# Kernel optimization log

Measured on AMD Instinct MI355X. Metric: run time of the kernel, lower is better.

The kernel has to match this reference:

```python
import jax, jax.numpy as jnp
import numpy as np

N = 100000   # nodes
E = 1600000  # edges
IN = 128     # in_feats
H = 3        # num_heads
D = 16       # out_feats per head
K = 3        # hops
NEG_SLOPE = 0.2
EPS = 1e-9


def leaky(x):
    return jnp.where(x >= 0, x, NEG_SLOPE * x)


def segment_softmax(e, idx, n):
    # e: [E, H] scores, softmax over edges sharing the same idx (node)
    m = jax.ops.segment_max(e, idx, num_segments=n)
    ex = jnp.exp(e - m[idx])
    s = jax.ops.segment_sum(ex, idx, num_segments=n)
    return ex / s[idx]


def feat_trans(h, i, norm_scales, offsets, pos_emb):
    # per-hop mean/var normalization (biased var) + position embedding
    mean = h.mean(axis=-1, keepdims=True)
    var = h.var(axis=-1, keepdims=True) + EPS
    h = (h - mean) * norm_scales[i] * jax.lax.rsqrt(var) + offsets[i]
    return h + pos_emb[:, :, i, :]


def setup_inputs() -> dict:
    key = jax.random.key(0)
    ks = jax.random.split(key, 10)
    s = 0.1
    feat = jax.random.normal(ks[0], (N, IN), jnp.float32)
    src = jax.random.randint(ks[1], (E,), 0, N)
    dst = jax.random.randint(ks[2], (E,), 0, N)
    fc_W = jax.random.normal(ks[3], (IN, H * D), jnp.float32) * s
    attn_l = jax.random.normal(ks[4], (1, H, D), jnp.float32) * s
    attn_r = jax.random.normal(ks[5], (1, H, D), jnp.float32) * s
    hop_attn_l = jax.random.normal(ks[6], (1, H, D), jnp.float32) * s
    hop_attn_r = jax.random.normal(ks[7], (1, H, D), jnp.float32) * s
    pos_emb = jax.random.normal(ks[8], (1, H, K + 1, D), jnp.float32) * s
    norm_scales = jnp.ones((K + 1, 1, H, D), jnp.float32)
    offsets = jnp.zeros((K + 1, 1, H, D), jnp.float32)
    bias = jnp.zeros((H * D,), jnp.float32)
    return dict(feat=feat, src=src, dst=dst, fc_W=fc_W, attn_l=attn_l,
                attn_r=attn_r, hop_attn_l=hop_attn_l, hop_attn_r=hop_attn_r,
                pos_emb=pos_emb, norm_scales=norm_scales, offsets=offsets,
                bias=bias)


def reference(feat, src, dst, fc_W, attn_l, attn_r, hop_attn_l, hop_attn_r,
              pos_emb, norm_scales, offsets, bias):
    ft = (feat @ fc_W).reshape(N, H, D)            # [N,H,D]
    el = (ft * attn_l).sum(-1)                      # [N,H]
    er = (ft * attn_r).sum(-1)                      # [N,H]
    e = leaky(el[src] + er[dst])                    # [E,H]
    a_dst = jnp.clip(segment_softmax(e, dst, N), EPS, None)
    a_src = jnp.clip(segment_softmax(e, src, N), EPS, None)
    a = jnp.sqrt(a_dst * a_src)                     # [E,H] symmetric attention

    h_query = feat_trans(ft, 0, norm_scales, offsets, pos_emb)[:, :, None, :]
    hstack = []
    cur = ft
    for k in range(1, K + 1):
        msg = cur[src] * a[:, :, None]              # [E,H,D]
        cur = jax.ops.segment_sum(msg, dst, num_segments=N)
        hstack.append(feat_trans(cur, k, norm_scales, offsets, pos_emb))
    hstack = jnp.stack(hstack, axis=2)              # [N,H,K,D]

    # hop attention (weight_style='HA')
    astack = (hstack * hop_attn_r[:, :, None, :]).sum(-1, keepdims=True) \
           + (h_query * hop_attn_l[:, :, None, :]).sum(-1, keepdims=True)
    astack = jax.nn.softmax(leaky(astack), axis=2)  # [N,H,K,1]
    rst = (hstack * astack).sum(axis=2)             # [N,H,D]
    return rst + bias.reshape(1, H, D)
```

## Files before the change

kernel.cpp:

```cpp
#include <hip/hip_runtime.h>
#include <hip/hip_bf16.h>

typedef __hip_bfloat16 bf16;

#define N_NODES 100000
#define N_EDGES 1600000
#define IN_F    128
#define HH      3
#define DD      16
#define HD      48
#define NEG_SLOPE 0.2f
#define EPS_V   1e-9f

#define NB      391
#define BW_SH   8
#define MS_T    8192

__device__ __forceinline__ float leaky(float x) { return x >= 0.f ? x : NEG_SLOPE * x; }
__device__ __forceinline__ float b2f(bf16 x) { return __bfloat162float(x); }

__global__ __launch_bounds__(256) void k_gemm(const float* __restrict__ feat,
                                              const float* __restrict__ W,
                                              float* __restrict__ ft,
                                              bf16* __restrict__ ft16) {
    int row = blockIdx.x * 256 + threadIdx.x;
    if (row >= N_NODES) return;
    float acc[HD];
#pragma unroll
    for (int c = 0; c < HD; ++c) acc[c] = 0.f;
    const float4* frow = (const float4*)(feat + (size_t)row * IN_F);
    for (int k4 = 0; k4 < IN_F / 4; ++k4) {
        float4 f = frow[k4];
        int k = k4 * 4;
#pragma unroll
        for (int c = 0; c < HD; ++c) acc[c] += f.x * W[(k + 0) * HD + c];
#pragma unroll
        for (int c = 0; c < HD; ++c) acc[c] += f.y * W[(k + 1) * HD + c];
#pragma unroll
        for (int c = 0; c < HD; ++c) acc[c] += f.z * W[(k + 2) * HD + c];
#pragma unroll
        for (int c = 0; c < HD; ++c) acc[c] += f.w * W[(k + 3) * HD + c];
    }
    float4* orow = (float4*)(ft + (size_t)row * HD);
#pragma unroll
    for (int c = 0; c < HD / 4; ++c)
        orow[c] = make_float4(acc[4 * c], acc[4 * c + 1], acc[4 * c + 2], acc[4 * c + 3]);
    bf16* o16 = ft16 + (size_t)row * HD;
#pragma unroll
    for (int c = 0; c < HD; ++c) o16[c] = __float2bfloat16(acc[c]);
}

__global__ void k_eler(const float* __restrict__ ft, const float* __restrict__ attn_l,
                       const float* __restrict__ attn_r, float* __restrict__ el,
                       float* __restrict__ er) {
    int i = blockIdx.x * blockDim.x + threadIdx.x;
    if (i >= N_NODES * HH) return;
    int h = i % HH;
    float sl = 0.f, sr = 0.f;
#pragma unroll
    for (int d = 0; d < DD; ++d) {
        float v = ft[i * DD + d];
        sl += v * attn_l[h * DD + d];
        sr += v * attn_r[h * DD + d];
    }
    el[i] = sl;
    er[i] = sr;
}

__global__ __launch_bounds__(256) void k_bhist(const int4* __restrict__ src4,
                                               const int4* __restrict__ dst4,
                                               int* __restrict__ bcnt_s,
                                               int* __restrict__ bcnt_d) {
    __shared__ int ls[NB], ld_[NB];
    int t = threadIdx.x;
    for (int i = t; i < NB; i += 256) { ls[i] = 0; ld_[i] = 0; }
    __syncthreads();
    const int NE4 = N_EDGES / 4;
    for (int e = blockIdx.x * 256 + t; e < NE4; e += gridDim.x * 256) {
        int4 d = dst4[e];
        atomicAdd(&ld_[d.x >> BW_SH], 1);
        atomicAdd(&ld_[d.y >> BW_SH], 1);
        atomicAdd(&ld_[d.z >> BW_SH], 1);
        atomicAdd(&ld_[d.w >> BW_SH], 1);
        int4 s = src4[e];
        atomicAdd(&ls[s.x >> BW_SH], 1);
        atomicAdd(&ls[s.y >> BW_SH], 1);
        atomicAdd(&ls[s.z >> BW_SH], 1);
        atomicAdd(&ls[s.w >> BW_SH], 1);
    }
    __syncthreads();
    for (int i = t; i < NB; i += 256) {
        if (ld_[i]) atomicAdd(&bcnt_d[i], ld_[i]);
        if (ls[i]) atomicAdd(&bcnt_s[i], ls[i]);
    }
}

__global__ __launch_bounds__(512) void k_bscan(const int* __restrict__ bcnt_d,
                                               int* __restrict__ bbase_d,
                                               const int* __restrict__ bcnt_s,
                                               int* __restrict__ bbase_s,
                                               int* __restrict__ rows_d,
                                               int* __restrict__ rows_s) {
    __shared__ int buf[512];
    const int* c = blockIdx.x ? bcnt_s : bcnt_d;
    int* o = blockIdx.x ? bbase_s : bbase_d;
    int t = threadIdx.x;
    int v = (t < NB) ? c[t] : 0;
    buf[t] = v;
    __syncthreads();
    for (int off = 1; off < 512; off <<= 1) {
        int u = (t >= off) ? buf[t - off] : 0;
        __syncthreads();
        buf[t] += u;
        __syncthreads();
    }
    if (t < NB) o[t] = buf[t] - v;
    if (t == NB - 1) o[NB] = buf[t];
    if (t == 0) {
        if (blockIdx.x) rows_s[N_NODES] = N_EDGES;
        else            rows_d[N_NODES] = N_EDGES;
    }
}

__global__ __launch_bounds__(256) void k_msplit(const int* __restrict__ src,
                                                const int* __restrict__ dst,
                                                const int* __restrict__ bbase_d,
                                                const int* __restrict__ bbase_s,
                                                int* __restrict__ bfill_d,
                                                int* __restrict__ bfill_s,
                                                unsigned* __restrict__ bkt_d,
                                                unsigned* __restrict__ bkt_s) {
    __shared__ int lcD[NB], lcS[NB], wbD[NB], wbS[NB], rkD[NB], rkS[NB];
    int t = threadIdx.x;
    int e0 = blockIdx.x * MS_T;
    int e1 = min(e0 + MS_T, N_EDGES);
    for (int i = t; i < NB; i += 256) { lcD[i] = 0; lcS[i] = 0; rkD[i] = 0; rkS[i] = 0; }
    __syncthreads();
    for (int e = e0 + t; e < e1; e += 256) {
        atomicAdd(&lcD[dst[e] >> BW_SH], 1);
        atomicAdd(&lcS[src[e] >> BW_SH], 1);
    }
    __syncthreads();
    for (int i = t; i < NB; i += 256) {
        wbD[i] = bbase_d[i] + (lcD[i] ? atomicAdd(&bfill_d[i], lcD[i]) : 0);
        wbS[i] = bbase_s[i] + (lcS[i] ? atomicAdd(&bfill_s[i], lcS[i]) : 0);
    }
    __syncthreads();
    for (int e = e0 + t; e < e1; e += 256) {
        int s = src[e], d = dst[e];
        int bd = d >> BW_SH, bs = s >> BW_SH;
        int rd = atomicAdd(&rkD[bd], 1);
        int rs = atomicAdd(&rkS[bs], 1);
        bkt_d[wbD[bd] + rd] = (unsigned)s | ((unsigned)(d & 255) << 17);
        bkt_s[wbS[bs] + rs] = (unsigned)d | ((unsigned)(s & 255) << 17);
    }
}

__global__ __launch_bounds__(256) void k_bfinal(const unsigned* __restrict__ bkt,
                                                const int* __restrict__ bbase,
                                                int* __restrict__ rows,
                                                int* __restrict__ outarr) {
    __shared__ int cnt[256], pre[256], rnk[256], wsum[4];
    int b = blockIdx.x, t = threadIdx.x;
    int base = bbase[b], end = bbase[b + 1];
    cnt[t] = 0; rnk[t] = 0;
    __syncthreads();
    for (int i = base + t; i < end; i += 256)
        atomicAdd(&cnt[(bkt[i] >> 17) & 255], 1);
    __syncthreads();
    int lane = t & 63, w = t >> 6;
    int v = cnt[t];
    int sc = v;
#pragma unroll
    for (int off = 1; off < 64; off <<= 1) {
        int u = __shfl_up(sc, off, 64);
        if (lane >= off) sc += u;
    }
    if (lane == 63) wsum[w] = sc;
    __syncthreads();
    int wpre = 0;
    for (int j = 0; j < w; ++j) wpre += wsum[j];
    int excl = wpre + sc - v;
    pre[t] = excl;
    int n = (b << BW_SH) + t;
    if (n < N_NODES) rows[n] = base + excl;
    __syncthreads();
    for (int i = base + t; i < end; i += 256) {
        unsigned u = bkt[i];
        int loc = (u >> 17) & 255;
        int r = atomicAdd(&rnk[loc], 1);
        outarr[base + pre[loc] + r] = (int)(u & 0x1FFFFu);
    }
}

__global__ __launch_bounds__(256) void k_seg_src(const int* __restrict__ dsts_s,
                                                 const int* __restrict__ rows_s,
                                                 const float* __restrict__ el,
                                                 const float* __restrict__ er,
                                                 float2* __restrict__ mssrc) {
    int wid = threadIdx.x >> 6, lane = threadIdx.x & 63;
    int n = blockIdx.x * 4 + wid;
    if (n >= N_NODES) return;
    int rs = rows_s[n], re = rows_s[n + 1];
    if (rs >= re) return;
    float el0 = el[n * 3 + 0], el1 = el[n * 3 + 1], el2 = el[n * 3 + 2];
    bool single = (re - rs) <= 64;
    float m0 = -INFINITY, m1 = -INFINITY, m2 = -INFINITY;
    float c0 = -INFINITY, c1 = -INFINITY, c2 = -INFINITY;
    for (int p0 = rs; p0 < re; p0 += 64) {
        int p = p0 + lane;
        bool act = p < re;
        int d = act ? dsts_s[p] : 0;
        float t0 = act ? leaky(el0 + er[d * 3 + 0]) : -INFINITY;
        float t1 = act ? leaky(el1 + er[d * 3 + 1]) : -INFINITY;
        float t2 = act ? leaky(el2 + er[d * 3 + 2]) : -INFINITY;
        if (single) { c0 = t0; c1 = t1; c2 = t2; }
        m0 = fmaxf(m0, t0); m1 = fmaxf(m1, t1); m2 = fmaxf(m2, t2);
    }
#pragma unroll
    for (int off = 1; off < 64; off <<= 1) {
        m0 = fmaxf(m0, __shfl_xor(m0, off));
        m1 = fmaxf(m1, __shfl_xor(m1, off));
        m2 = fmaxf(m2, __shfl_xor(m2, off));
    }
    float s0 = 0, s1 = 0, s2 = 0;
    if (single) {
        bool act = (rs + lane) < re;
        s0 = act ? expf(c0 - m0) : 0.f;
        s1 = act ? expf(c1 - m1) : 0.f;
        s2 = act ? expf(c2 - m2) : 0.f;
    } else {
        for (int p0 = rs; p0 < re; p0 += 64) {
            int p = p0 + lane;
            if (p < re) {
                int d = dsts_s[p];
                s0 += expf(leaky(el0 + er[d * 3 + 0]) - m0);
                s1 += expf(leaky(el1 + er[d * 3 + 1]) - m1);
                s2 += expf(leaky(el2 + er[d * 3 + 2]) - m2);
            }
        }
    }
#pragma unroll
    for (int off = 1; off < 64; off <<= 1) {
        s0 += __shfl_xor(s0, off);
        s1 += __shfl_xor(s1, off);
        s2 += __shfl_xor(s2, off);
    }
    if (lane == 0) {
        mssrc[n * 3 + 0] = make_float2(m0, s0);
        mssrc[n * 3 + 1] = make_float2(m1, s1);
        mssrc[n * 3 + 2] = make_float2(m2, s2);
    }
}

__global__ __launch_bounds__(256) void k_seg_dst_attn(const int* __restrict__ srcs_d,
                                                      const int* __restrict__ rows_d,
                                                      const float* __restrict__ el,
                                                      const float* __restrict__ er,
                                                      const float2* __restrict__ mssrc,
                                                      float* __restrict__ a_sorted) {
    int wid = threadIdx.x >> 6, lane = threadIdx.x & 63;
    int n = blockIdx.x * 4 + wid;
    if (n >= N_NODES) return;
    int rs = rows_d[n], re = rows_d[n + 1];
    if (rs >= re) return;
    float er0 = er[n * 3 + 0], er1 = er[n * 3 + 1], er2 = er[n * 3 + 2];
    bool single = (re - rs) <= 64;
    float m0 = -INFINITY, m1 = -INFINITY, m2 = -INFINITY;
    float c0 = -INFINITY, c1 = -INFINITY, c2 = -INFINITY;
    int scache = 0;
    for (int p0 = rs; p0 < re; p0 += 64) {
        int p = p0 + lane;
        bool act = p < re;
        int s = act ? srcs_d[p] : 0;
        if (single) scache = s;
        float t0 = act ? leaky(el[s * 3 + 0] + er0) : -INFINITY;
        float t1 = act ? leaky(el[s * 3 + 1] + er1) : -INFINITY;
        float t2 = act ? leaky(el[s * 3 + 2] + er2) : -INFINITY;
        if (single) { c0 = t0; c1 = t1; c2 = t2; }
        m0 = fmaxf(m0, t0); m1 = fmaxf(m1, t1); m2 = fmaxf(m2, t2);
    }
#pragma unroll
    for (int off = 1; off < 64; off <<= 1) {
        m0 = fmaxf(m0, __shfl_xor(m0, off));
        m1 = fmaxf(m1, __shfl_xor(m1, off));
        m2 = fmaxf(m2, __shfl_xor(m2, off));
    }
    float s0 = 0, s1 = 0, s2 = 0;
    if (single) {
        bool act = (rs + lane) < re;
        s0 = act ? expf(c0 - m0) : 0.f;
        s1 = act ? expf(c1 - m1) : 0.f;
        s2 = act ? expf(c2 - m2) : 0.f;
    } else {
        for (int p0 = rs; p0 < re; p0 += 64) {
            int p = p0 + lane;
            if (p < re) {
                int s = srcs_d[p];
                s0 += expf(leaky(el[s * 3 + 0] + er0) - m0);
                s1 += expf(leaky(el[s * 3 + 1] + er1) - m1);
                s2 += expf(leaky(el[s * 3 + 2] + er2) - m2);
            }
        }
    }
#pragma unroll
    for (int off = 1; off < 64; off <<= 1) {
        s0 += __shfl_xor(s0, off);
        s1 += __shfl_xor(s1, off);
        s2 += __shfl_xor(s2, off);
    }
    float i0 = 1.f / s0, i1 = 1.f / s1, i2 = 1.f / s2;
    for (int p0 = rs; p0 < re; p0 += 64) {
        int p = p0 + lane;
        if (p >= re) break;
        int s = single ? scache : srcs_d[p];
        float t0, t1, t2;
        if (single) { t0 = c0; t1 = c1; t2 = c2; }
        else {
            t0 = leaky(el[s * 3 + 0] + er0);
            t1 = leaky(el[s * 3 + 1] + er1);
            t2 = leaky(el[s * 3 + 2] + er2);
        }
        float2 a0 = mssrc[s * 3 + 0], a1 = mssrc[s * 3 + 1], a2 = mssrc[s * 3 + 2];
        float d0 = fmaxf(expf(t0 - m0) * i0, EPS_V);
        float d1 = fmaxf(expf(t1 - m1) * i1, EPS_V);
        float d2 = fmaxf(expf(t2 - m2) * i2, EPS_V);
        float u0 = fmaxf(expf(t0 - a0.x) / a0.y, EPS_V);
        float u1 = fmaxf(expf(t1 - a1.x) / a1.y, EPS_V);
        float u2 = fmaxf(expf(t2 - a2.x) / a2.y, EPS_V);
        a_sorted[p * 3 + 0] = sqrtf(d0 * u0);
        a_sorted[p * 3 + 1] = sqrtf(d1 * u1);
        a_sorted[p * 3 + 2] = sqrtf(d2 * u2);
    }
}

__global__ __launch_bounds__(256) void k_hop(const bf16* __restrict__ cur,
                                             const float* __restrict__ a_sorted,
                                             const int* __restrict__ rowstart,
                                             const int* __restrict__ src_sorted,
                                             bf16* __restrict__ out) {
    int wid = threadIdx.x >> 6, lane = threadIdx.x & 63;
    int n = blockIdx.x * 4 + wid;
    if (n >= N_NODES) return;
    if (lane >= HD) return;
    int h = lane >> 4;
    int rs = rowstart[n], re = rowstart[n + 1];
    float acc = 0.f;
    int p = rs;
    for (; p + 8 <= re; p += 8) {
        int s[8];
#pragma unroll
        for (int j = 0; j < 8; ++j) s[j] = src_sorted[p + j];
        float a[8];
#pragma unroll
        for (int j = 0; j < 8; ++j) a[j] = a_sorted[(p + j) * HH + h];
        float v[8];
#pragma unroll
        for (int j = 0; j < 8; ++j) v[j] = b2f(cur[s[j] * HD + lane]);
#pragma unroll
        for (int j = 0; j < 8; ++j) acc += a[j] * v[j];
    }
    if (p < re) {
        int cnt = re - p;
        int s[8];
#pragma unroll
        for (int j = 0; j < 8; ++j) s[j] = (j < cnt) ? src_sorted[p + j] : 0;
        float a[8];
#pragma unroll
        for (int j = 0; j < 8; ++j) a[j] = (j < cnt) ? a_sorted[(p + j) * HH + h] : 0.f;
        float v[8];
#pragma unroll
        for (int j = 0; j < 8; ++j) v[j] = (j < cnt) ? b2f(cur[s[j] * HD + lane]) : 0.f;
#pragma unroll
        for (int j = 0; j < 8; ++j) acc += a[j] * v[j];
    }
    out[n * HD + lane] = __float2bfloat16(acc);
}

__global__ void k_final(const float* __restrict__ ft, const bf16* __restrict__ cur1,
                        const bf16* __restrict__ cur2, const bf16* __restrict__ cur3,
                        const float* __restrict__ hop_l, const float* __restrict__ hop_r,
                        const float* __restrict__ pos_emb, const float* __restrict__ scales,
                        const float* __restrict__ offs, const float* __restrict__ bias,
                        float* __restrict__ out) {
    int i = blockIdx.x * blockDim.x + threadIdx.x;
    if (i >= N_NODES * HH) return;
    int h = i % HH;
    float hk[4][DD];
#pragma unroll
    for (int k = 0; k < 4; ++k) {
        float x[DD];
#pragma unroll
        for (int d = 0; d < DD; ++d) {
            x[d] = (k == 0) ? ft[(size_t)i * DD + d]
                 : (k == 1) ? b2f(cur1[(size_t)i * DD + d])
                 : (k == 2) ? b2f(cur2[(size_t)i * DD + d])
                            : b2f(cur3[(size_t)i * DD + d]);
        }
        float m = 0.f;
#pragma unroll
        for (int d = 0; d < DD; ++d) m += x[d];
        m *= (1.f / DD);
        float v2 = 0.f;
#pragma unroll
        for (int d = 0; d < DD; ++d) {
            float c = x[d] - m;
            v2 += c * c;
        }
        v2 = v2 * (1.f / DD) + EPS_V;
        float rsq = rsqrtf(v2);
#pragma unroll
        for (int d = 0; d < DD; ++d) {
            hk[k][d] = (x[d] - m) * scales[k * HD + h * DD + d] * rsq +
                       offs[k * HD + h * DD + d] + pos_emb[h * 64 + k * DD + d];
        }
    }
    float al = 0.f;
#pragma unroll
    for (int d = 0; d < DD; ++d) al += hk[0][d] * hop_l[h * DD + d];
    float ar[3], mx = -1e30f;
#pragma unroll
    for (int k = 0; k < 3; ++k) {
        float s = 0.f;
#pragma unroll
        for (int d = 0; d < DD; ++d) s += hk[k + 1][d] * hop_r[h * DD + d];
        ar[k] = leaky(s + al);
        mx = fmaxf(mx, ar[k]);
    }
    float den = 0.f, wgt[3];
#pragma unroll
    for (int k = 0; k < 3; ++k) {
        wgt[k] = expf(ar[k] - mx);
        den += wgt[k];
    }
#pragma unroll
    for (int k = 0; k < 3; ++k) wgt[k] /= den;
#pragma unroll
    for (int d = 0; d < DD; ++d) {
        float o = hk[1][d] * wgt[0] + hk[2][d] * wgt[1] + hk[3][d] * wgt[2] +
                  bias[h * DD + d];
        out[i * DD + d] = o;
    }
}

#define OFF_FT     0u
#define OFF_FT16   4800000u
#define OFF_EL     7200000u
#define OFF_ER     7500000u
#define OFF_MSSRC  7800000u
#define OFF_BCNT   8400000u
#define OFF_BBASE  8401600u
#define OFF_ROWD   8402400u
#define OFF_ROWS_  8502402u
#define OFF_BKTD   8602404u
#define OFF_BKTS   10202404u
#define OFF_SRCSD  11802404u
#define OFF_DSTSS  13402404u
#define OFF_ASORT  15002404u
#define OFF_CUR1   19802404u
#define OFF_CUR2   22202404u
#define OFF_CUR3   24602404u
#define WS_FLOATS  27002404u

extern "C" void kernel_launch(void* const* d_in, const int* in_sizes, int n_in,
                              void* d_out, int out_size, void* d_ws, size_t ws_size,
                              hipStream_t stream) {
    if (ws_size < (size_t)WS_FLOATS * 4) return;

    const float* feat   = (const float*)d_in[0];
    const int*   src    = (const int*)d_in[1];
    const int*   dst    = (const int*)d_in[2];
    const float* fc_W   = (const float*)d_in[3];
    const float* attn_l = (const float*)d_in[4];
    const float* attn_r = (const float*)d_in[5];
    const float* hop_l  = (const float*)d_in[6];
    const float* hop_r  = (const float*)d_in[7];
    const float* pos    = (const float*)d_in[8];
    const float* scal   = (const float*)d_in[9];
    const float* offs   = (const float*)d_in[10];
    const float* bias   = (const float*)d_in[11];
    float* out = (float*)d_out;

    float* ws = (float*)d_ws;
    float*    ft      = ws + OFF_FT;
    bf16*     ft16    = (bf16*)(ws + OFF_FT16);
    float*    el      = ws + OFF_EL;
    float*    er      = ws + OFF_ER;
    float2*   mssrc   = (float2*)(ws + OFF_MSSRC);
    int*      bcnt_d  = (int*)(ws + OFF_BCNT);
    int*      bcnt_s  = bcnt_d + 400;
    int*      bfill_d = bcnt_d + 800;
    int*      bfill_s = bcnt_d + 1200;
    int*      bbase_d = (int*)(ws + OFF_BBASE);
    int*      bbase_s = bbase_d + 400;
    int*      rows_d  = (int*)(ws + OFF_ROWD);
    int*      rows_s  = (int*)(ws + OFF_ROWS_);
    unsigned* bkt_d   = (unsigned*)(ws + OFF_BKTD);
    unsigned* bkt_s   = (unsigned*)(ws + OFF_BKTS);
    int*      srcs_d  = (int*)(ws + OFF_SRCSD);
    int*      dsts_s  = (int*)(ws + OFF_DSTSS);
    float*    a_sorted= ws + OFF_ASORT;
    bf16*     cur1    = (bf16*)(ws + OFF_CUR1);
    bf16*     cur2    = (bf16*)(ws + OFF_CUR2);
    bf16*     cur3    = (bf16*)(ws + OFF_CUR3);

    hipMemsetAsync(ws + OFF_BCNT, 0, 1600 * 4, stream);

    k_gemm<<<(N_NODES + 255) / 256, 256, 0, stream>>>(feat, fc_W, ft, ft16);
    k_eler<<<(N_NODES * HH + 255) / 256, 256, 0, stream>>>(ft, attn_l, attn_r, el, er);

    k_bhist<<<400, 256, 0, stream>>>((const int4*)src, (const int4*)dst, bcnt_s, bcnt_d);
    k_bscan<<<2, 512, 0, stream>>>(bcnt_d, bbase_d, bcnt_s, bbase_s, rows_d, rows_s);
    k_msplit<<<(N_EDGES + MS_T - 1) / MS_T, 256, 0, stream>>>(src, dst, bbase_d, bbase_s,
                                                              bfill_d, bfill_s, bkt_d, bkt_s);
    k_bfinal<<<NB, 256, 0, stream>>>(bkt_d, bbase_d, rows_d, srcs_d);
    k_bfinal<<<NB, 256, 0, stream>>>(bkt_s, bbase_s, rows_s, dsts_s);

    k_seg_src<<<(N_NODES + 3) / 4, 256, 0, stream>>>(dsts_s, rows_s, el, er, mssrc);
    k_seg_dst_attn<<<(N_NODES + 3) / 4, 256, 0, stream>>>(srcs_d, rows_d, el, er,
                                                          mssrc, a_sorted);
    k_hop<<<(N_NODES + 3) / 4, 256, 0, stream>>>(ft16, a_sorted, rows_d, srcs_d, cur1);
    k_hop<<<(N_NODES + 3) / 4, 256, 0, stream>>>(cur1, a_sorted, rows_d, srcs_d, cur2);
    k_hop<<<(N_NODES + 3) / 4, 256, 0, stream>>>(cur2, a_sorted, rows_d, srcs_d, cur3);
    k_final<<<(N_NODES * HH + 255) / 256, 256, 0, stream>>>(ft, cur1, cur2, cur3, hop_l,
                                                            hop_r, pos, scal, offs, bias,
                                                            out);
}
```

Measured before the change: 493.6 us.

## Switch hop SpMM to head-major layout with thread-per-node-head gathers

Stores bf16 features and edge attention in head-major planes ([H][N][16] and [H][E]). The hop kernel now uses one thread per (node, head), gathering each neighbor's 16-value head slice with two 16-byte loads and accumulating 16 outputs in registers. Before, a 64-lane wavefront per node used only 48 lanes, each doing scalar bf16 loads. The change aims to use every lane and cut per-element load instructions. In exchange, lanes in a wave now walk different nodes' edge lists, so loop trip counts and srcs/attention reads are no longer coalesced or uniform across the wave.

```diff
diff --git a/kernel.cpp b/kernel.cpp
--- a/kernel.cpp
+++ b/kernel.cpp
@@ -18,6 +18,11 @@
 
 __device__ __forceinline__ float leaky(float x) { return x >= 0.f ? x : NEG_SLOPE * x; }
 __device__ __forceinline__ float b2f(bf16 x) { return __bfloat162float(x); }
+__device__ __forceinline__ unsigned pkbf(float a, float b) {
+    unsigned ua = (unsigned)__builtin_bit_cast(unsigned short, __float2bfloat16(a));
+    unsigned ub = (unsigned)__builtin_bit_cast(unsigned short, __float2bfloat16(b));
+    return ua | (ub << 16);
+}
 
 __global__ __launch_bounds__(256) void k_gemm(const float* __restrict__ feat,
                                               const float* __restrict__ W,
@@ -45,9 +50,21 @@
 #pragma unroll
     for (int c = 0; c < HD / 4; ++c)
         orow[c] = make_float4(acc[4 * c], acc[4 * c + 1], acc[4 * c + 2], acc[4 * c + 3]);
-    bf16* o16 = ft16 + (size_t)row * HD;
-#pragma unroll
-    for (int c = 0; c < HD; ++c) o16[c] = __float2bfloat16(acc[c]);
+#pragma unroll
+    for (int hh = 0; hh < HH; ++hh) {
+        uint4 w0, w1;
+        w0.x = pkbf(acc[hh * 16 + 0], acc[hh * 16 + 1]);
+        w0.y = pkbf(acc[hh * 16 + 2], acc[hh * 16 + 3]);
+        w0.z = pkbf(acc[hh * 16 + 4], acc[hh * 16 + 5]);
+        w0.w = pkbf(acc[hh * 16 + 6], acc[hh * 16 + 7]);
+        w1.x = pkbf(acc[hh * 16 + 8], acc[hh * 16 + 9]);
+        w1.y = pkbf(acc[hh * 16 + 10], acc[hh * 16 + 11]);
+        w1.z = pkbf(acc[hh * 16 + 12], acc[hh * 16 + 13]);
+        w1.w = pkbf(acc[hh * 16 + 14], acc[hh * 16 + 15]);
+        uint4* o = (uint4*)(ft16 + ((size_t)hh * N_NODES + row) * 16);
+        o[0] = w0;
+        o[1] = w1;
+    }
 }
 
 __global__ void k_eler(const float* __restrict__ ft, const float* __restrict__ attn_l,
@@ -258,7 +275,7 @@
                                                       const float* __restrict__ el,
                                                       const float* __restrict__ er,
                                                       const float2* __restrict__ mssrc,
-                                                      float* __restrict__ a_sorted) {
+                                                      float* __restrict__ a_h) {
     int wid = threadIdx.x >> 6, lane = threadIdx.x & 63;
     int n = blockIdx.x * 4 + wid;
     if (n >= N_NODES) return;
@@ -328,53 +345,71 @@
         float u0 = fmaxf(expf(t0 - a0.x) / a0.y, EPS_V);
         float u1 = fmaxf(expf(t1 - a1.x) / a1.y, EPS_V);
         float u2 = fmaxf(expf(t2 - a2.x) / a2.y, EPS_V);
-        a_sorted[p * 3 + 0] = sqrtf(d0 * u0);
-        a_sorted[p * 3 + 1] = sqrtf(d1 * u1);
-        a_sorted[p * 3 + 2] = sqrtf(d2 * u2);
+        a_h[0 * N_EDGES + p] = sqrtf(d0 * u0);
+        a_h[1 * N_EDGES + p] = sqrtf(d1 * u1);
+        a_h[2 * N_EDGES + p] = sqrtf(d2 * u2);
     }
 }
 
 __global__ __launch_bounds__(256) void k_hop(const bf16* __restrict__ cur,
-                                             const float* __restrict__ a_sorted,
-                                             const int* __restrict__ rowstart,
-                                             const int* __restrict__ src_sorted,
+                                             const float* __restrict__ a_h,
+                                             const int* __restrict__ rows_d,
+                                             const int* __restrict__ srcs_d,
                                              bf16* __restrict__ out) {
-    int wid = threadIdx.x >> 6, lane = threadIdx.x & 63;
-    int n = blockIdx.x * 4 + wid;
-    if (n >= N_NODES) return;
-    if (lane >= HD) return;
-    int h = lane >> 4;
-    int rs = rowstart[n], re = rowstart[n + 1];
-    float acc = 0.f;
-    int p = rs;
-    for (; p + 8 <= re; p += 8) {
-        int s[8];
-#pragma unroll
-        for (int j = 0; j < 8; ++j) s[j] = src_sorted[p + j];
-        float a[8];
-#pragma unroll
-        for (int j = 0; j < 8; ++j) a[j] = a_sorted[(p + j) * HH + h];
-        float v[8];
-#pragma unroll
-        for (int j = 0; j < 8; ++j) v[j] = b2f(cur[s[j] * HD + lane]);
-#pragma unroll
-        for (int j = 0; j < 8; ++j) acc += a[j] * v[j];
-    }
-    if (p < re) {
+    int i = blockIdx.x * 256 + threadIdx.x;
+    if (i >= HH * N_NODES) return;
+    int h = i / N_NODES;
+    int n = i - h * N_NODES;
+    int rs = rows_d[n], re = rows_d[n + 1];
+    const float* ah = a_h + (size_t)h * N_EDGES;
+    const bf16* curh = cur + (size_t)h * N_NODES * 16;
+    float acc[16];
+#pragma unroll
+    for (int d = 0; d < 16; ++d) acc[d] = 0.f;
+    for (int p = rs; p < re; p += 8) {
         int cnt = re - p;
         int s[8];
-#pragma unroll
-        for (int j = 0; j < 8; ++j) s[j] = (j < cnt) ? src_sorted[p + j] : 0;
         float a[8];
 #pragma unroll
-        for (int j = 0; j < 8; ++j) a[j] = (j < cnt) ? a_sorted[(p + j) * HH + h] : 0.f;
-        float v[8];
-#pragma unroll
-        for (int j = 0; j < 8; ++j) v[j] = (j < cnt) ? b2f(cur[s[j] * HD + lane]) : 0.f;
-#pragma unroll
-        for (int j = 0; j < 8; ++j) acc += a[j] * v[j];
-    }
-    out[n * HD + lane] = __float2bfloat16(acc);
+        for (int j = 0; j < 8; ++j) s[j] = (j < cnt) ? srcs_d[p + j] : 0;
+#pragma unroll
+        for (int j = 0; j < 8; ++j) a[j] = (j < cnt) ? ah[p + j] : 0.f;
+        uint4 g0[8], g1[8];
+#pragma unroll
+        for (int j = 0; j < 8; ++j) {
+            const uint4* cp = (const uint4*)(curh + (size_t)s[j] * 16);
+            g0[j] = cp[0];
+            g1[j] = cp[1];
+        }
+#pragma unroll
+        for (int j = 0; j < 8; ++j) {
+            unsigned u;
+            u = g0[j].x; acc[0]  += a[j] * __uint_as_float(u << 16);
+                         acc[1]  += a[j] * __uint_as_float(u & 0xffff0000u);
+            u = g0[j].y; acc[2]  += a[j] * __uint_as_float(u << 16);
+                         acc[3]  += a[j] * __uint_as_float(u & 0xffff0000u);
+            u = g0[j].z; acc[4]  += a[j] * __uint_as_float(u << 16);
+                         acc[5]  += a[j] * __uint_as_float(u & 0xffff0000u);
+            u = g0[j].w; acc[6]  += a[j] * __uint_as_float(u << 16);
+                         acc[7]  += a[j] * __uint_as_float(u & 0xffff0000u);
+            u = g1[j].x; acc[8]  += a[j] * __uint_as_float(u << 16);
+                         acc[9]  += a[j] * __uint_as_float(u & 0xffff0000u);
+            u = g1[j].y; acc[10] += a[j] * __uint_as_float(u << 16);
+                         acc[11] += a[j] * __uint_as_float(u & 0xffff0000u);
+            u = g1[j].z; acc[12] += a[j] * __uint_as_float(u << 16);
+                         acc[13] += a[j] * __uint_as_float(u & 0xffff0000u);
+            u = g1[j].w; acc[14] += a[j] * __uint_as_float(u << 16);
+                         acc[15] += a[j] * __uint_as_float(u & 0xffff0000u);
+        }
+    }
+    uint4 w0, w1;
+    w0.x = pkbf(acc[0], acc[1]);   w0.y = pkbf(acc[2], acc[3]);
+    w0.z = pkbf(acc[4], acc[5]);   w0.w = pkbf(acc[6], acc[7]);
+    w1.x = pkbf(acc[8], acc[9]);   w1.y = pkbf(acc[10], acc[11]);
+    w1.z = pkbf(acc[12], acc[13]); w1.w = pkbf(acc[14], acc[15]);
+    uint4* o = (uint4*)(out + (size_t)i * 16);
+    o[0] = w0;
+    o[1] = w1;
 }
 
 __global__ void k_final(const float* __restrict__ ft, const bf16* __restrict__ cur1,
@@ -386,6 +421,8 @@
     int i = blockIdx.x * blockDim.x + threadIdx.x;
     if (i >= N_NODES * HH) return;
     int h = i % HH;
+    int n = i / HH;
+    size_t sl = ((size_t)h * N_NODES + n) * 16;
     float hk[4][DD];
 #pragma unroll
     for (int k = 0; k < 4; ++k) {
@@ -393,9 +430,9 @@
 #pragma unroll
         for (int d = 0; d < DD; ++d) {
             x[d] = (k == 0) ? ft[(size_t)i * DD + d]
-                 : (k == 1) ? b2f(cur1[(size_t)i * DD + d])
-                 : (k == 2) ? b2f(cur2[(size_t)i * DD + d])
-                            : b2f(cur3[(size_t)i * DD + d]);
+                 : (k == 1) ? b2f(cur1[sl + d])
+                 : (k == 2) ? b2f(cur2[sl + d])
+                            : b2f(cur3[sl + d]);
         }
         float m = 0.f;
 #pragma unroll
@@ -499,7 +536,7 @@
     unsigned* bkt_s   = (unsigned*)(ws + OFF_BKTS);
     int*      srcs_d  = (int*)(ws + OFF_SRCSD);
     int*      dsts_s  = (int*)(ws + OFF_DSTSS);
-    float*    a_sorted= ws + OFF_ASORT;
+    float*    a_h     = ws + OFF_ASORT;
     bf16*     cur1    = (bf16*)(ws + OFF_CUR1);
     bf16*     cur2    = (bf16*)(ws + OFF_CUR2);
     bf16*     cur3    = (bf16*)(ws + OFF_CUR3);
@@ -518,10 +555,11 @@
 
     k_seg_src<<<(N_NODES + 3) / 4, 256, 0, stream>>>(dsts_s, rows_s, el, er, mssrc);
     k_seg_dst_attn<<<(N_NODES + 3) / 4, 256, 0, stream>>>(srcs_d, rows_d, el, er,
-                                                          mssrc, a_sorted);
-    k_hop<<<(N_NODES + 3) / 4, 256, 0, stream>>>(ft16, a_sorted, rows_d, srcs_d, cur1);
-    k_hop<<<(N_NODES + 3) / 4, 256, 0, stream>>>(cur1, a_sorted, rows_d, srcs_d, cur2);
-    k_hop<<<(N_NODES + 3) / 4, 256, 0, stream>>>(cur2, a_sorted, rows_d, srcs_d, cur3);
+                                                          mssrc, a_h);
+    const int HOPG = (HH * N_NODES + 255) / 256;
+    k_hop<<<HOPG, 256, 0, stream>>>(ft16, a_h, rows_d, srcs_d, cur1);
+    k_hop<<<HOPG, 256, 0, stream>>>(cur1, a_h, rows_d, srcs_d, cur2);
+    k_hop<<<HOPG, 256, 0, stream>>>(cur2, a_h, rows_d, srcs_d, cur3);
     k_final<<<(N_NODES * HH + 255) / 256, 256, 0, stream>>>(ft, cur1, cur2, cur3, hop_l,
                                                             hop_r, pos, scal, offs, bias,
                                                             out);
```

After: 624.5 us. +26.5%, slower.

## Drop fp32 ft copy, store attention as head-major bf16 arrays

Applied to the files above, without the earlier changes.

The GEMM now writes only a bf16 copy of ft, using packed 16-byte stores. k_eler and k_final read that bf16 copy through vector unpacking instead of the fp32 array. Edge attention weights are stored as bf16 in a head-major [H][E] layout rather than fp32 [E][H], which cuts the bytes k_hop reads per edge and makes those reads contiguous. The trade-off is lower precision in el/er, in the hop-0 normalization input and in the attention coefficients.

```diff
diff --git a/kernel.cpp b/kernel.cpp
--- a/kernel.cpp
+++ b/kernel.cpp
@@ -18,10 +18,17 @@
 
 __device__ __forceinline__ float leaky(float x) { return x >= 0.f ? x : NEG_SLOPE * x; }
 __device__ __forceinline__ float b2f(bf16 x) { return __bfloat162float(x); }
+__device__ __forceinline__ unsigned short bfbits(float x) {
+    return __builtin_bit_cast(unsigned short, __float2bfloat16(x));
+}
+__device__ __forceinline__ unsigned pkbf(float a, float b) {
+    return (unsigned)bfbits(a) | ((unsigned)bfbits(b) << 16);
+}
+__device__ __forceinline__ float ulo(unsigned u) { return __uint_as_float(u << 16); }
+__device__ __forceinline__ float uhi(unsigned u) { return __uint_as_float(u & 0xffff0000u); }
 
 __global__ __launch_bounds__(256) void k_gemm(const float* __restrict__ feat,
                                               const float* __restrict__ W,
-                                              float* __restrict__ ft,
                                               bf16* __restrict__ ft16) {
     int row = blockIdx.x * 256 + threadIdx.x;
     if (row >= N_NODES) return;
@@ -41,27 +48,36 @@
 #pragma unroll
         for (int c = 0; c < HD; ++c) acc[c] += f.w * W[(k + 3) * HD + c];
     }
-    float4* orow = (float4*)(ft + (size_t)row * HD);
-#pragma unroll
-    for (int c = 0; c < HD / 4; ++c)
-        orow[c] = make_float4(acc[4 * c], acc[4 * c + 1], acc[4 * c + 2], acc[4 * c + 3]);
-    bf16* o16 = ft16 + (size_t)row * HD;
-#pragma unroll
-    for (int c = 0; c < HD; ++c) o16[c] = __float2bfloat16(acc[c]);
-}
-
-__global__ void k_eler(const float* __restrict__ ft, const float* __restrict__ attn_l,
+    uint4* o16 = (uint4*)(ft16 + (size_t)row * HD);
+#pragma unroll
+    for (int q = 0; q < 6; ++q) {
+        uint4 w;
+        w.x = pkbf(acc[q * 8 + 0], acc[q * 8 + 1]);
+        w.y = pkbf(acc[q * 8 + 2], acc[q * 8 + 3]);
+        w.z = pkbf(acc[q * 8 + 4], acc[q * 8 + 5]);
+        w.w = pkbf(acc[q * 8 + 6], acc[q * 8 + 7]);
+        o16[q] = w;
+    }
+}
+
+__global__ void k_eler(const bf16* __restrict__ ft16, const float* __restrict__ attn_l,
                        const float* __restrict__ attn_r, float* __restrict__ el,
                        float* __restrict__ er) {
     int i = blockIdx.x * blockDim.x + threadIdx.x;
     if (i >= N_NODES * HH) return;
     int h = i % HH;
+    const uint4* p = (const uint4*)(ft16 + (size_t)i * DD);
+    uint4 q0 = p[0], q1 = p[1];
+    float x[DD];
+    x[0] = ulo(q0.x);  x[1] = uhi(q0.x);  x[2] = ulo(q0.y);  x[3] = uhi(q0.y);
+    x[4] = ulo(q0.z);  x[5] = uhi(q0.z);  x[6] = ulo(q0.w);  x[7] = uhi(q0.w);
+    x[8] = ulo(q1.x);  x[9] = uhi(q1.x);  x[10] = ulo(q1.y); x[11] = uhi(q1.y);
+    x[12] = ulo(q1.z); x[13] = uhi(q1.z); x[14] = ulo(q1.w); x[15] = uhi(q1.w);
     float sl = 0.f, sr = 0.f;
 #pragma unroll
     for (int d = 0; d < DD; ++d) {
-        float v = ft[i * DD + d];
-        sl += v * attn_l[h * DD + d];
-        sr += v * attn_r[h * DD + d];
+        sl += x[d] * attn_l[h * DD + d];
+        sr += x[d] * attn_r[h * DD + d];
     }
     el[i] = sl;
     er[i] = sr;
@@ -258,7 +274,7 @@
                                                       const float* __restrict__ el,
                                                       const float* __restrict__ er,
                                                       const float2* __restrict__ mssrc,
-                                                      float* __restrict__ a_sorted) {
+                                                      bf16* __restrict__ a16) {
     int wid = threadIdx.x >> 6, lane = threadIdx.x & 63;
     int n = blockIdx.x * 4 + wid;
     if (n >= N_NODES) return;
@@ -328,35 +344,36 @@
         float u0 = fmaxf(expf(t0 - a0.x) / a0.y, EPS_V);
         float u1 = fmaxf(expf(t1 - a1.x) / a1.y, EPS_V);
         float u2 = fmaxf(expf(t2 - a2.x) / a2.y, EPS_V);
-        a_sorted[p * 3 + 0] = sqrtf(d0 * u0);
-        a_sorted[p * 3 + 1] = sqrtf(d1 * u1);
-        a_sorted[p * 3 + 2] = sqrtf(d2 * u2);
+        a16[0 * (size_t)N_EDGES + p] = __float2bfloat16(sqrtf(d0 * u0));
+        a16[1 * (size_t)N_EDGES + p] = __float2bfloat16(sqrtf(d1 * u1));
+        a16[2 * (size_t)N_EDGES + p] = __float2bfloat16(sqrtf(d2 * u2));
     }
 }
 
 __global__ __launch_bounds__(256) void k_hop(const bf16* __restrict__ cur,
-                                             const float* __restrict__ a_sorted,
-                                             const int* __restrict__ rowstart,
-                                             const int* __restrict__ src_sorted,
+                                             const bf16* __restrict__ a16,
+                                             const int* __restrict__ rows_d,
+                                             const int* __restrict__ srcs_d,
                                              bf16* __restrict__ out) {
     int wid = threadIdx.x >> 6, lane = threadIdx.x & 63;
     int n = blockIdx.x * 4 + wid;
     if (n >= N_NODES) return;
     if (lane >= HD) return;
     int h = lane >> 4;
-    int rs = rowstart[n], re = rowstart[n + 1];
+    const bf16* ah = a16 + (size_t)h * N_EDGES;
+    int rs = rows_d[n], re = rows_d[n + 1];
     float acc = 0.f;
     int p = rs;
     for (; p + 8 <= re; p += 8) {
         int s[8];
 #pragma unroll
-        for (int j = 0; j < 8; ++j) s[j] = src_sorted[p + j];
+        for (int j = 0; j < 8; ++j) s[j] = srcs_d[p + j];
         float a[8];
 #pragma unroll
-        for (int j = 0; j < 8; ++j) a[j] = a_sorted[(p + j) * HH + h];
+        for (int j = 0; j < 8; ++j) a[j] = b2f(ah[p + j]);
         float v[8];
 #pragma unroll
-        for (int j = 0; j < 8; ++j) v[j] = b2f(cur[s[j] * HD + lane]);
+        for (int j = 0; j < 8; ++j) v[j] = b2f(cur[(size_t)s[j] * HD + lane]);
 #pragma unroll
         for (int j = 0; j < 8; ++j) acc += a[j] * v[j];
     }
@@ -364,20 +381,29 @@
         int cnt = re - p;
         int s[8];
 #pragma unroll
-        for (int j = 0; j < 8; ++j) s[j] = (j < cnt) ? src_sorted[p + j] : 0;
+        for (int j = 0; j < 8; ++j) s[j] = (j < cnt) ? srcs_d[p + j] : 0;
         float a[8];
 #pragma unroll
-        for (int j = 0; j < 8; ++j) a[j] = (j < cnt) ? a_sorted[(p + j) * HH + h] : 0.f;
+        for (int j = 0; j < 8; ++j) a[j] = (j < cnt) ? b2f(ah[p + j]) : 0.f;
         float v[8];
 #pragma unroll
-        for (int j = 0; j < 8; ++j) v[j] = (j < cnt) ? b2f(cur[s[j] * HD + lane]) : 0.f;
+        for (int j = 0; j < 8; ++j) v[j] = (j < cnt) ? b2f(cur[(size_t)s[j] * HD + lane]) : 0.f;
 #pragma unroll
         for (int j = 0; j < 8; ++j) acc += a[j] * v[j];
     }
-    out[n * HD + lane] = __float2bfloat16(acc);
-}
-
-__global__ void k_final(const float* __restrict__ ft, const bf16* __restrict__ cur1,
+    out[(size_t)n * HD + lane] = __float2bfloat16(acc);
+}
+
+__device__ __forceinline__ void unpack16(const bf16* p, float* x) {
+    const uint4* q = (const uint4*)p;
+    uint4 q0 = q[0], q1 = q[1];
+    x[0] = ulo(q0.x);  x[1] = uhi(q0.x);  x[2] = ulo(q0.y);  x[3] = uhi(q0.y);
+    x[4] = ulo(q0.z);  x[5] = uhi(q0.z);  x[6] = ulo(q0.w);  x[7] = uhi(q0.w);
+    x[8] = ulo(q1.x);  x[9] = uhi(q1.x);  x[10] = ulo(q1.y); x[11] = uhi(q1.y);
+    x[12] = ulo(q1.z); x[13] = uhi(q1.z); x[14] = ulo(q1.w); x[15] = uhi(q1.w);
+}
+
+__global__ void k_final(const bf16* __restrict__ ft16, const bf16* __restrict__ cur1,
                         const bf16* __restrict__ cur2, const bf16* __restrict__ cur3,
                         const float* __restrict__ hop_l, const float* __restrict__ hop_r,
                         const float* __restrict__ pos_emb, const float* __restrict__ scales,
@@ -386,17 +412,14 @@
     int i = blockIdx.x * blockDim.x + threadIdx.x;
     if (i >= N_NODES * HH) return;
     int h = i % HH;
+    int n = i / HH;
+    size_t sl = (size_t)n * HD + h * DD;
     float hk[4][DD];
 #pragma unroll
     for (int k = 0; k < 4; ++k) {
         float x[DD];
-#pragma unroll
-        for (int d = 0; d < DD; ++d) {
-            x[d] = (k == 0) ? ft[(size_t)i * DD + d]
-                 : (k == 1) ? b2f(cur1[(size_t)i * DD + d])
-                 : (k == 2) ? b2f(cur2[(size_t)i * DD + d])
-                            : b2f(cur3[(size_t)i * DD + d]);
-        }
+        unpack16((k == 0) ? ft16 + sl : (k == 1) ? cur1 + sl : (k == 2) ? cur2 + sl
+                                                                        : cur3 + sl, x);
         float m = 0.f;
 #pragma unroll
         for (int d = 0; d < DD; ++d) m += x[d];
@@ -443,24 +466,23 @@
     }
 }
 
-#define OFF_FT     0u
-#define OFF_FT16   4800000u
-#define OFF_EL     7200000u
-#define OFF_ER     7500000u
-#define OFF_MSSRC  7800000u
-#define OFF_BCNT   8400000u
-#define OFF_BBASE  8401600u
-#define OFF_ROWD   8402400u
-#define OFF_ROWS_  8502402u
-#define OFF_BKTD   8602404u
-#define OFF_BKTS   10202404u
-#define OFF_SRCSD  11802404u
-#define OFF_DSTSS  13402404u
-#define OFF_ASORT  15002404u
-#define OFF_CUR1   19802404u
-#define OFF_CUR2   22202404u
-#define OFF_CUR3   24602404u
-#define WS_FLOATS  27002404u
+#define OFF_FT16   0u
+#define OFF_EL     2400000u
+#define OFF_ER     2700000u
+#define OFF_MSSRC  3000000u
+#define OFF_BCNT   3600000u
+#define OFF_BBASE  3601600u
+#define OFF_ROWD   3602400u
+#define OFF_ROWS_  3702402u
+#define OFF_BKTD   3802404u
+#define OFF_BKTS   5402404u
+#define OFF_SRCSD  7002404u
+#define OFF_DSTSS  8602404u
+#define OFF_A16    10202404u
+#define OFF_CUR1   12602404u
+#define OFF_CUR2   15002404u
+#define OFF_CUR3   17402404u
+#define WS_FLOATS  19802404u
 
 extern "C" void kernel_launch(void* const* d_in, const int* in_sizes, int n_in,
                               void* d_out, int out_size, void* d_ws, size_t ws_size,
@@ -482,7 +504,6 @@
     float* out = (float*)d_out;
 
     float* ws = (float*)d_ws;
-    float*    ft      = ws + OFF_FT;
     bf16*     ft16    = (bf16*)(ws + OFF_FT16);
     float*    el      = ws + OFF_EL;
     float*    er      = ws + OFF_ER;
@@ -499,15 +520,15 @@
     unsigned* bkt_s   = (unsigned*)(ws + OFF_BKTS);
     int*      srcs_d  = (int*)(ws + OFF_SRCSD);
     int*      dsts_s  = (int*)(ws + OFF_DSTSS);
-    float*    a_sorted= ws + OFF_ASORT;
+    bf16*     a16     = (bf16*)(ws + OFF_A16);
     bf16*     cur1    = (bf16*)(ws + OFF_CUR1);
     bf16*     cur2    = (bf16*)(ws + OFF_CUR2);
     bf16*     cur3    = (bf16*)(ws + OFF_CUR3);
 
     hipMemsetAsync(ws + OFF_BCNT, 0, 1600 * 4, stream);
 
-    k_gemm<<<(N_NODES + 255) / 256, 256, 0, stream>>>(feat, fc_W, ft, ft16);
-    k_eler<<<(N_NODES * HH + 255) / 256, 256, 0, stream>>>(ft, attn_l, attn_r, el, er);
+    k_gemm<<<(N_NODES + 255) / 256, 256, 0, stream>>>(feat, fc_W, ft16);
+    k_eler<<<(N_NODES * HH + 255) / 256, 256, 0, stream>>>(ft16, attn_l, attn_r, el, er);
 
     k_bhist<<<400, 256, 0, stream>>>((const int4*)src, (const int4*)dst, bcnt_s, bcnt_d);
     k_bscan<<<2, 512, 0, stream>>>(bcnt_d, bbase_d, bcnt_s, bbase_s, rows_d, rows_s);
@@ -518,11 +539,11 @@
 
     k_seg_src<<<(N_NODES + 3) / 4, 256, 0, stream>>>(dsts_s, rows_s, el, er, mssrc);
     k_seg_dst_attn<<<(N_NODES + 3) / 4, 256, 0, stream>>>(srcs_d, rows_d, el, er,
-                                                          mssrc, a_sorted);
-    k_hop<<<(N_NODES + 3) / 4, 256, 0, stream>>>(ft16, a_sorted, rows_d, srcs_d, cur1);
-    k_hop<<<(N_NODES + 3) / 4, 256, 0, stream>>>(cur1, a_sorted, rows_d, srcs_d, cur2);
-    k_hop<<<(N_NODES + 3) / 4, 256, 0, stream>>>(cur2, a_sorted, rows_d, srcs_d, cur3);
-    k_final<<<(N_NODES * HH + 255) / 256, 256, 0, stream>>>(ft, cur1, cur2, cur3, hop_l,
+                                                          mssrc, a16);
+    k_hop<<<(N_NODES + 3) / 4, 256, 0, stream>>>(ft16, a16, rows_d, srcs_d, cur1);
+    k_hop<<<(N_NODES + 3) / 4, 256, 0, stream>>>(cur1, a16, rows_d, srcs_d, cur2);
+    k_hop<<<(N_NODES + 3) / 4, 256, 0, stream>>>(cur2, a16, rows_d, srcs_d, cur3);
+    k_final<<<(N_NODES * HH + 255) / 256, 256, 0, stream>>>(ft16, cur1, cur2, cur3, hop_l,
                                                             hop_r, pos, scal, offs, bias,
                                                             out);
 }
```

New measurement: 546.1 us. +10.6%, slower.
